# Kernel tuning notes

Hardware: AMD Instinct MI355X
Metric: run time of the kernel (lower is better)

Reference implementation:

```python
import jax, jax.numpy as jnp
import numpy as np

N = 100000
E = 1600000
F_IN = 128
HID1, H1 = 32, 4
HID2, H2 = 32, 4
NUM_CLASSES = 16
NEG_SLOPE = 0.2  # PyG GATConv default


def _glorot(key, shape, fan_in):
    return jax.random.normal(key, shape, dtype=jnp.float32) / jnp.sqrt(jnp.float32(fan_in))


def setup_inputs() -> dict:
    key = jax.random.key(0)
    ks = jax.random.split(key, 12)
    x = jax.random.normal(ks[0], (N, F_IN), dtype=jnp.float32)
    edge_index = jax.random.randint(ks[1], (2, E), 0, N, dtype=jnp.int64)
    W1 = _glorot(ks[2], (F_IN, H1 * HID1), F_IN)
    a_src1 = _glorot(ks[3], (H1, HID1), HID1)
    a_dst1 = _glorot(ks[4], (H1, HID1), HID1)
    b1 = jnp.zeros((H1 * HID1,), dtype=jnp.float32)
    W2 = _glorot(ks[5], (H1 * HID1, H2 * HID2), H1 * HID1)
    a_src2 = _glorot(ks[6], (H2, HID2), HID2)
    a_dst2 = _glorot(ks[7], (H2, HID2), HID2)
    b2 = jnp.zeros((HID2,), dtype=jnp.float32)
    Wc = _glorot(ks[8], (HID2, NUM_CLASSES), HID2)
    bc = jnp.zeros((NUM_CLASSES,), dtype=jnp.float32)
    return {"x": x, "edge_index": edge_index, "W1": W1, "a_src1": a_src1,
            "a_dst1": a_dst1, "b1": b1, "W2": W2, "a_src2": a_src2,
            "a_dst2": a_dst2, "b2": b2, "Wc": Wc, "bc": bc}


def gat_layer(x, src, dst, W, a_s, a_d, b, concat):
    # x: [N, Fin]; src/dst: [E'] with self-loops included
    n = x.shape[0]
    H, C = a_s.shape
    h = (x @ W).reshape(n, H, C)                      # [N, H, C]
    alpha_s = jnp.einsum('nhc,hc->nh', h, a_s)        # [N, H]
    alpha_d = jnp.einsum('nhc,hc->nh', h, a_d)
    e = jax.nn.leaky_relu(alpha_s[src] + alpha_d[dst], NEG_SLOPE)  # [E', H]
    m = jax.ops.segment_max(e, dst, num_segments=n)   # segment softmax (stable)
    ex = jnp.exp(e - m[dst])
    denom = jax.ops.segment_sum(ex, dst, num_segments=n)
    alpha = ex / denom[dst]                           # [E', H]
    msg = alpha[:, :, None] * h[src]                  # [E', H, C]
    out = jax.ops.segment_sum(msg, dst, num_segments=n)  # [N, H, C]
    out = out.reshape(n, H * C) if concat else out.mean(axis=1)
    return out + b


def reference(x, edge_index, W1, a_src1, a_dst1, b1, W2, a_src2, a_dst2, b2, Wc, bc):
    n = x.shape[0]
    loop = jnp.arange(n, dtype=edge_index.dtype)
    src = jnp.concatenate([edge_index[0], loop])  # add self-loops (PyG default)
    dst = jnp.concatenate([edge_index[1], loop])
    h = gat_layer(x, src, dst, W1, a_src1, a_dst1, b1, concat=True)
    h = jax.nn.relu(h)  # dropout is identity in eval mode
    h = gat_layer(h, src, dst, W2, a_src2, a_dst2, b2, concat=False)
    h = jax.nn.relu(h)
    return h @ Wc + bc
```

## Files before the change

### kernel.cpp

```cpp
#include <hip/hip_runtime.h>
#include <hip/hip_fp16.h>


__device__ __forceinline__ float leaky02(float v) { return v > 0.f ? v : 0.2f * v; }

struct h2x2 { __half2 a, b; };

#define NPB 1024
#define MAXNB 128
#define EPT 16
#define CH 4096

__global__ __launch_bounds__(256) void k_bucketize(const int* __restrict__ ei,
                                                   uint2* __restrict__ ebuf,
                                                   int* __restrict__ bcur,
                                                   int E, int N, int NB, int region) {
  __shared__ int hist[MAXNB];
  __shared__ int lbase[MAXNB];
  const int t = threadIdx.x;
  const int base = blockIdx.x * CH;
  const int Ep = E + N;
  if (t < MAXNB) hist[t] = 0;
  __syncthreads();
  int src[EPT], dst[EPT];
#pragma unroll
  for (int k = 0; k < EPT; ++k) {
    int e = base + k * 256 + t;
    if (e < E) { src[k] = ei[e]; dst[k] = ei[E + e]; }
    else if (e < Ep) { src[k] = dst[k] = e - E; }
    else { src[k] = -1; dst[k] = -1; }
    if (dst[k] >= 0) atomicAdd(&hist[dst[k] >> 10], 1);
  }
  __syncthreads();
  if (t < NB && hist[t] > 0) lbase[t] = atomicAdd(&bcur[t], hist[t]);
  __syncthreads();
  if (t < MAXNB) hist[t] = 0;
  __syncthreads();
#pragma unroll
  for (int k = 0; k < EPT; ++k) {
    if (dst[k] >= 0) {
      int b = dst[k] >> 10;
      int r = atomicAdd(&hist[b], 1);
      ebuf[(size_t)b * region + lbase[b] + r] =
          make_uint2((unsigned)src[k], (unsigned)dst[k]);
    }
  }
}

__global__ void k_bscan(const int* __restrict__ bcur, int* __restrict__ colbase,
                        int* __restrict__ rowptr, int NB, int N, int Ep) {
  __shared__ int lds[MAXNB];
  int t = threadIdx.x;
  int v = (t < NB) ? bcur[t] : 0;
  lds[t] = v;
  __syncthreads();
  for (int off = 1; off < MAXNB; off <<= 1) {
    int u = (t >= off) ? lds[t - off] : 0;
    __syncthreads();
    lds[t] += u;
    __syncthreads();
  }
  if (t < NB) colbase[t] = lds[t] - v;
  if (t == 0) rowptr[N] = Ep;
}

__global__ __launch_bounds__(256) void k_csr(const uint2* __restrict__ ebuf,
                                             const int* __restrict__ bcur,
                                             const int* __restrict__ colbase,
                                             int* __restrict__ rowptr,
                                             int* __restrict__ colsrc,
                                             int N, int region) {
  __shared__ int cnt[NPB];
  __shared__ int lds2[256];
  const int b = blockIdx.x;
  const int t = threadIdx.x;
  const int m = bcur[b];
  const size_t ebase = (size_t)b * region;
  const int cb = colbase[b];
#pragma unroll
  for (int i = 0; i < 4; ++i) cnt[t * 4 + i] = 0;
  __syncthreads();
  for (int j = t; j < m; j += 256) {
    int d = (int)(ebuf[ebase + j].y) & (NPB - 1);
    atomicAdd(&cnt[d], 1);
  }
  __syncthreads();
  int v[4], s = 0;
#pragma unroll
  for (int i = 0; i < 4; ++i) { v[i] = cnt[t * 4 + i]; s += v[i]; }
  lds2[t] = s;
  __syncthreads();
  for (int off = 1; off < 256; off <<= 1) {
    int u = (t >= off) ? lds2[t - off] : 0;
    __syncthreads();
    lds2[t] += u;
    __syncthreads();
  }
  int e = lds2[t] - s;
  const int node0 = (b << 10) + t * 4;
#pragma unroll
  for (int i = 0; i < 4; ++i) {
    cnt[t * 4 + i] = e;
    if (node0 + i < N) rowptr[node0 + i] = cb + e;
    e += v[i];
  }
  __syncthreads();
  for (int j = t; j < m; j += 256) {
    uint2 q = ebuf[ebase + j];
    int d = (int)q.y & (NPB - 1);
    int r = atomicAdd(&cnt[d], 1);
    colsrc[cb + r] = (int)q.x;
  }
}

__global__ __launch_bounds__(256) void k_gemm_fused(const float* __restrict__ A,
                                                    const float* __restrict__ W,
                                                    const float* __restrict__ avs,
                                                    const float* __restrict__ avd,
                                                    __half* __restrict__ Hh,
                                                    float* __restrict__ as_out,
                                                    float* __restrict__ ad_out,
                                                    int nrows) {
  __shared__ float sA[16][68];
  __shared__ float sB[16][68];
  const int t = threadIdx.x;
  const int row0 = blockIdx.x * 64;
  const int col0 = blockIdx.y * 64;
  const int tx = t & 15, ty = t >> 4;
  float acc[4][4] = {{0.f, 0.f, 0.f, 0.f}, {0.f, 0.f, 0.f, 0.f},
                     {0.f, 0.f, 0.f, 0.f}, {0.f, 0.f, 0.f, 0.f}};
  for (int kc = 0; kc < 128; kc += 16) {
    {
      int m = t >> 2;
      int k4 = (t & 3) * 4;
      int row = row0 + m;
      float4 a = (row < nrows) ? *(const float4*)&A[(size_t)row * 128 + kc + k4]
                               : make_float4(0.f, 0.f, 0.f, 0.f);
      sA[k4 + 0][m] = a.x;
      sA[k4 + 1][m] = a.y;
      sA[k4 + 2][m] = a.z;
      sA[k4 + 3][m] = a.w;
    }
    {
      int kk = t >> 4;
      int c4 = (t & 15) * 4;
      float4 b = *(const float4*)&W[(size_t)(kc + kk) * 128 + col0 + c4];
      *(float4*)&sB[kk][c4] = b;
    }
    __syncthreads();
#pragma unroll
    for (int k = 0; k < 16; ++k) {
      const float4 a = *(const float4*)&sA[k][ty * 4];
      const float4 b = *(const float4*)&sB[k][tx * 4];
      float av[4] = {a.x, a.y, a.z, a.w};
      float bv[4] = {b.x, b.y, b.z, b.w};
#pragma unroll
      for (int i = 0; i < 4; ++i)
#pragma unroll
        for (int j = 0; j < 4; ++j) acc[i][j] = fmaf(av[i], bv[j], acc[i][j]);
    }
    __syncthreads();
  }
  const float4 s4 = *(const float4*)&avs[col0 + tx * 4];
  const float4 d4 = *(const float4*)&avd[col0 + tx * 4];
#pragma unroll
  for (int i = 0; i < 4; ++i) {
    const int row = row0 + ty * 4 + i;
    float ps = acc[i][0] * s4.x + acc[i][1] * s4.y + acc[i][2] * s4.z + acc[i][3] * s4.w;
    float pd = acc[i][0] * d4.x + acc[i][1] * d4.y + acc[i][2] * d4.z + acc[i][3] * d4.w;
    for (int off = 1; off < 8; off <<= 1) {
      ps += __shfl_xor(ps, off);
      pd += __shfl_xor(pd, off);
    }
    if (row < nrows) {
      if ((tx & 7) == 0) {
        int head = (col0 >> 5) + (tx >> 3);
        as_out[row * 4 + head] = ps;
        ad_out[row * 4 + head] = pd;
      }
      h2x2 pk;
      pk.a = __floats2half2_rn(acc[i][0], acc[i][1]);
      pk.b = __floats2half2_rn(acc[i][2], acc[i][3]);
      *(h2x2*)&Hh[(size_t)row * 128 + col0 + tx * 4] = pk;
    }
  }
}

template <int LAYER>
__global__ __launch_bounds__(256) void k_agg(const int* __restrict__ rowptr,
                                             const int* __restrict__ colsrc,
                                             const float* __restrict__ as,
                                             const float* __restrict__ ad,
                                             const __half* __restrict__ Hh,
                                             const float* __restrict__ b1,
                                             const float* __restrict__ b2,
                                             const float* __restrict__ Wc,
                                             const float* __restrict__ bc,
                                             float* __restrict__ out, int n) {
  __shared__ float sbuf[8][128];
  const int slot = threadIdx.x >> 5;
  const int l = threadIdx.x & 31;
  const int node = blockIdx.x * 8 + slot;
  const bool active = node < n;
  int start = 0, end = 0;
  float4 adv = make_float4(0.f, 0.f, 0.f, 0.f);
  if (active) {
    start = rowptr[node];
    end = rowptr[node + 1];
    adv = *(const float4*)&ad[node * 4];
  }
  const int hd = l >> 3;
  const float adh = hd == 0 ? adv.x : hd == 1 ? adv.y : hd == 2 ? adv.z : adv.w;
  const int c = l * 4;
  float4 acc = make_float4(0.f, 0.f, 0.f, 0.f);
  float dsum = 0.f;
  int e = start;
  for (; e + 3 < end; e += 4) {
    int s0 = colsrc[e], s1 = colsrc[e + 1], s2 = colsrc[e + 2], s3 = colsrc[e + 3];
    float a0 = as[s0 * 4 + hd];
    float a1 = as[s1 * 4 + hd];
    float a2 = as[s2 * 4 + hd];
    float a3 = as[s3 * 4 + hd];
    h2x2 q0 = *(const h2x2*)&Hh[(size_t)s0 * 128 + c];
    h2x2 q1 = *(const h2x2*)&Hh[(size_t)s1 * 128 + c];
    h2x2 q2 = *(const h2x2*)&Hh[(size_t)s2 * 128 + c];
    h2x2 q3 = *(const h2x2*)&Hh[(size_t)s3 * 128 + c];
    float w0 = __expf(leaky02(a0 + adh));
    float w1 = __expf(leaky02(a1 + adh));
    float w2 = __expf(leaky02(a2 + adh));
    float w3 = __expf(leaky02(a3 + adh));
    dsum += w0 + w1 + w2 + w3;
    float2 f0a = __half22float2(q0.a), f0b = __half22float2(q0.b);
    float2 f1a = __half22float2(q1.a), f1b = __half22float2(q1.b);
    float2 f2a = __half22float2(q2.a), f2b = __half22float2(q2.b);
    float2 f3a = __half22float2(q3.a), f3b = __half22float2(q3.b);
    acc.x = fmaf(w0, f0a.x, acc.x); acc.y = fmaf(w0, f0a.y, acc.y);
    acc.z = fmaf(w0, f0b.x, acc.z); acc.w = fmaf(w0, f0b.y, acc.w);
    acc.x = fmaf(w1, f1a.x, acc.x); acc.y = fmaf(w1, f1a.y, acc.y);
    acc.z = fmaf(w1, f1b.x, acc.z); acc.w = fmaf(w1, f1b.y, acc.w);
    acc.x = fmaf(w2, f2a.x, acc.x); acc.y = fmaf(w2, f2a.y, acc.y);
    acc.z = fmaf(w2, f2b.x, acc.z); acc.w = fmaf(w2, f2b.y, acc.w);
    acc.x = fmaf(w3, f3a.x, acc.x); acc.y = fmaf(w3, f3a.y, acc.y);
    acc.z = fmaf(w3, f3b.x, acc.z); acc.w = fmaf(w3, f3b.y, acc.w);
  }
  for (; e < end; ++e) {
    int s0 = colsrc[e];
    float w = __expf(leaky02(as[s0 * 4 + hd] + adh));
    h2x2 q = *(const h2x2*)&Hh[(size_t)s0 * 128 + c];
    float2 fa = __half22float2(q.a), fb = __half22float2(q.b);
    dsum += w;
    acc.x = fmaf(w, fa.x, acc.x); acc.y = fmaf(w, fa.y, acc.y);
    acc.z = fmaf(w, fb.x, acc.z); acc.w = fmaf(w, fb.y, acc.w);
  }
  const float inv = dsum > 0.f ? 1.0f / dsum : 0.f;
  acc.x *= inv; acc.y *= inv; acc.z *= inv; acc.w *= inv;
  if (LAYER == 1) {
    if (active) {
      float4 bv = *(const float4*)&b1[c];
      acc.x = fmaxf(acc.x + bv.x, 0.f);
      acc.y = fmaxf(acc.y + bv.y, 0.f);
      acc.z = fmaxf(acc.z + bv.z, 0.f);
      acc.w = fmaxf(acc.w + bv.w, 0.f);
      *(float4*)&out[(size_t)node * 128 + c] = acc;
    }
  } else {
    *(float4*)&sbuf[slot][c] = acc;
    __syncthreads();
    float f = 0.25f * (sbuf[slot][l] + sbuf[slot][l + 32] +
                       sbuf[slot][l + 64] + sbuf[slot][l + 96]);
    f = fmaxf(f + b2[l], 0.f);
    __syncthreads();
    sbuf[slot][l] = f;
    __syncthreads();
    if (active && l < 16) {
      float o = bc[l];
#pragma unroll
      for (int cc = 0; cc < 32; ++cc) o = fmaf(sbuf[slot][cc], Wc[cc * 16 + l], o);
      out[(size_t)node * 16 + l] = o;
    }
  }
}

extern "C" void kernel_launch(void* const* d_in, const int* in_sizes, int n_in,
                              void* d_out, int out_size, void* d_ws, size_t ws_size,
                              hipStream_t stream) {
  const float* x = (const float*)d_in[0];
  const int* ei = (const int*)d_in[1];
  const float* W1 = (const float*)d_in[2];
  const float* a_s1 = (const float*)d_in[3];
  const float* a_d1 = (const float*)d_in[4];
  const float* b1 = (const float*)d_in[5];
  const float* W2 = (const float*)d_in[6];
  const float* a_s2 = (const float*)d_in[7];
  const float* a_d2 = (const float*)d_in[8];
  const float* b2 = (const float*)d_in[9];
  const float* Wc = (const float*)d_in[10];
  const float* bc = (const float*)d_in[11];
  float* out = (float*)d_out;

  const int N = in_sizes[0] / 128;
  const int E = in_sizes[1] / 2;
  const int Ep = E + N;
  const int NB = (N + NPB - 1) >> 10;
  const int region = Ep / NB + 4096;

  char* p = (char*)d_ws;
  auto align16 = [](char* q) { return (char*)(((uintptr_t)q + 15) & ~(uintptr_t)15); };
  __half* Hh = (__half*)p;            p = align16(p + sizeof(__half) * (size_t)N * 128);
  float* x2 = (float*)p;              p = align16(p + sizeof(float) * (size_t)N * 128);
  float* asb = (float*)p;             p = align16(p + sizeof(float) * (size_t)N * 4);
  float* adb = (float*)p;             p = align16(p + sizeof(float) * (size_t)N * 4);
  int* rowptr = (int*)p;              p = align16(p + sizeof(int) * (size_t)(N + 1));
  int* bcur = (int*)p;                p = align16(p + sizeof(int) * MAXNB);
  int* colbase = (int*)p;             p = align16(p + sizeof(int) * MAXNB);
  int* colsrc = (int*)p;              p = align16(p + sizeof(int) * (size_t)Ep);
  uint2* ebuf = (uint2*)p;

  hipMemsetAsync(bcur, 0, sizeof(int) * MAXNB, stream);

  k_bucketize<<<(Ep + CH - 1) / CH, 256, 0, stream>>>(ei, ebuf, bcur, E, N, NB, region);
  k_bscan<<<1, MAXNB, 0, stream>>>(bcur, colbase, rowptr, NB, N, Ep);
  k_csr<<<NB, 256, 0, stream>>>(ebuf, bcur, colbase, rowptr, colsrc, N, region);

  dim3 ggrid((N + 63) / 64, 2);
  k_gemm_fused<<<ggrid, 256, 0, stream>>>(x, W1, a_s1, a_d1, Hh, asb, adb, N);
  k_agg<1><<<(N + 7) / 8, 256, 0, stream>>>(rowptr, colsrc, asb, adb, Hh,
                                            b1, nullptr, nullptr, nullptr, x2, N);
  k_gemm_fused<<<ggrid, 256, 0, stream>>>(x2, W2, a_s2, a_d2, Hh, asb, adb, N);
  k_agg<2><<<(N + 7) / 8, 256, 0, stream>>>(rowptr, colsrc, asb, adb, Hh,
                                            nullptr, b2, Wc, bc, out, N);
}
```

Baseline: 429.2 us.

## Use fp16 MFMA GEMM, store layer-1 output in fp16, fold bucket scan into CSR

Replaces the fp32 SIMT tiled GEMM with a 16x16x32 fp16 MFMA kernel. Each block now covers all 128 output columns, with W transposed into LDS and the attention projections computed from the MFMA accumulators. The layer-1 aggregation writes its activations as fp16, which halves intermediate traffic and feeds the second GEMM directly. The separate bucket-scan kernel is merged into each CSR block, which removes one launch but makes every block redundantly redo the scan. The GEMM inputs are now rounded to fp16, which reduces precision.

Result: faster. 403.3 us (-6.0%).

```diff
diff --git a/kernel.cpp b/kernel.cpp
--- a/kernel.cpp
+++ b/kernel.cpp
@@ -1,6 +1,10 @@
 #include <hip/hip_runtime.h>
 #include <hip/hip_fp16.h>
 
+
+typedef _Float16 f16;
+typedef f16 f16x8 __attribute__((ext_vector_type(8)));
+typedef float f32x4 __attribute__((ext_vector_type(4)));
 
 __device__ __forceinline__ float leaky02(float v) { return v > 0.f ? v : 0.2f * v; }
 
@@ -47,36 +51,28 @@
   }
 }
 
-__global__ void k_bscan(const int* __restrict__ bcur, int* __restrict__ colbase,
-                        int* __restrict__ rowptr, int NB, int N, int Ep) {
-  __shared__ int lds[MAXNB];
-  int t = threadIdx.x;
-  int v = (t < NB) ? bcur[t] : 0;
-  lds[t] = v;
-  __syncthreads();
-  for (int off = 1; off < MAXNB; off <<= 1) {
-    int u = (t >= off) ? lds[t - off] : 0;
-    __syncthreads();
-    lds[t] += u;
-    __syncthreads();
-  }
-  if (t < NB) colbase[t] = lds[t] - v;
-  if (t == 0) rowptr[N] = Ep;
-}
-
 __global__ __launch_bounds__(256) void k_csr(const uint2* __restrict__ ebuf,
                                              const int* __restrict__ bcur,
-                                             const int* __restrict__ colbase,
                                              int* __restrict__ rowptr,
                                              int* __restrict__ colsrc,
-                                             int N, int region) {
+                                             int N, int NB, int region) {
   __shared__ int cnt[NPB];
   __shared__ int lds2[256];
+  __shared__ int sscan[MAXNB];
   const int b = blockIdx.x;
   const int t = threadIdx.x;
+  if (t < MAXNB) sscan[t] = (t < NB) ? bcur[t] : 0;
+  __syncthreads();
+  for (int off = 1; off < MAXNB; off <<= 1) {
+    int u = (t < MAXNB && t >= off) ? sscan[t - off] : 0;
+    __syncthreads();
+    if (t < MAXNB) sscan[t] += u;
+    __syncthreads();
+  }
+  const int cb = (b == 0) ? 0 : sscan[b - 1];
+  if (b == 0 && t == 0) rowptr[N] = sscan[NB - 1];
   const int m = bcur[b];
   const size_t ebase = (size_t)b * region;
-  const int cb = colbase[b];
 #pragma unroll
   for (int i = 0; i < 4; ++i) cnt[t * 4 + i] = 0;
   __syncthreads();
@@ -113,75 +109,106 @@
   }
 }
 
-__global__ __launch_bounds__(256) void k_gemm_fused(const float* __restrict__ A,
-                                                    const float* __restrict__ W,
-                                                    const float* __restrict__ avs,
-                                                    const float* __restrict__ avd,
-                                                    __half* __restrict__ Hh,
-                                                    float* __restrict__ as_out,
-                                                    float* __restrict__ ad_out,
-                                                    int nrows) {
-  __shared__ float sA[16][68];
-  __shared__ float sB[16][68];
+template <int AFP16>
+__global__ __launch_bounds__(256) void k_gemm_mfma(const void* __restrict__ Ain,
+                                                   const float* __restrict__ W,
+                                                   const float* __restrict__ avs,
+                                                   const float* __restrict__ avd,
+                                                   __half* __restrict__ Hh,
+                                                   float* __restrict__ as_out,
+                                                   float* __restrict__ ad_out,
+                                                   int nrows) {
+  __shared__ __align__(16) f16 sA[64][136];
+  __shared__ __align__(16) f16 sBT[128][136];
   const int t = threadIdx.x;
   const int row0 = blockIdx.x * 64;
-  const int col0 = blockIdx.y * 64;
-  const int tx = t & 15, ty = t >> 4;
-  float acc[4][4] = {{0.f, 0.f, 0.f, 0.f}, {0.f, 0.f, 0.f, 0.f},
-                     {0.f, 0.f, 0.f, 0.f}, {0.f, 0.f, 0.f, 0.f}};
-  for (int kc = 0; kc < 128; kc += 16) {
-    {
-      int m = t >> 2;
-      int k4 = (t & 3) * 4;
-      int row = row0 + m;
-      float4 a = (row < nrows) ? *(const float4*)&A[(size_t)row * 128 + kc + k4]
-                               : make_float4(0.f, 0.f, 0.f, 0.f);
-      sA[k4 + 0][m] = a.x;
-      sA[k4 + 1][m] = a.y;
-      sA[k4 + 2][m] = a.z;
-      sA[k4 + 3][m] = a.w;
-    }
-    {
-      int kk = t >> 4;
-      int c4 = (t & 15) * 4;
-      float4 b = *(const float4*)&W[(size_t)(kc + kk) * 128 + col0 + c4];
-      *(float4*)&sB[kk][c4] = b;
-    }
-    __syncthreads();
-#pragma unroll
-    for (int k = 0; k < 16; ++k) {
-      const float4 a = *(const float4*)&sA[k][ty * 4];
-      const float4 b = *(const float4*)&sB[k][tx * 4];
-      float av[4] = {a.x, a.y, a.z, a.w};
-      float bv[4] = {b.x, b.y, b.z, b.w};
-#pragma unroll
-      for (int i = 0; i < 4; ++i)
-#pragma unroll
-        for (int j = 0; j < 4; ++j) acc[i][j] = fmaf(av[i], bv[j], acc[i][j]);
-    }
-    __syncthreads();
-  }
-  const float4 s4 = *(const float4*)&avs[col0 + tx * 4];
-  const float4 d4 = *(const float4*)&avd[col0 + tx * 4];
-#pragma unroll
-  for (int i = 0; i < 4; ++i) {
-    const int row = row0 + ty * 4 + i;
-    float ps = acc[i][0] * s4.x + acc[i][1] * s4.y + acc[i][2] * s4.z + acc[i][3] * s4.w;
-    float pd = acc[i][0] * d4.x + acc[i][1] * d4.y + acc[i][2] * d4.z + acc[i][3] * d4.w;
-    for (int off = 1; off < 8; off <<= 1) {
-      ps += __shfl_xor(ps, off);
-      pd += __shfl_xor(pd, off);
+#pragma unroll
+  for (int i = 0; i < 16; ++i) {
+    int idx = (t + i * 256) * 4;
+    int k = idx >> 7, n = idx & 127;
+    float4 w4 = *(const float4*)&W[idx];
+    sBT[n + 0][k] = (f16)w4.x;
+    sBT[n + 1][k] = (f16)w4.y;
+    sBT[n + 2][k] = (f16)w4.z;
+    sBT[n + 3][k] = (f16)w4.w;
+  }
+  if (AFP16) {
+    const __half* A = (const __half*)Ain + (size_t)row0 * 128;
+#pragma unroll
+    for (int i = 0; i < 8; ++i) {
+      int idx = (t + i * 256) * 4;
+      int m = idx >> 7, c = idx & 127;
+      h2x2 v;
+      if (row0 + m < nrows) v = *(const h2x2*)&A[idx];
+      else { v.a = __floats2half2_rn(0.f, 0.f); v.b = v.a; }
+      *(h2x2*)&sA[m][c] = v;
+    }
+  } else {
+    const float* A = (const float*)Ain + (size_t)row0 * 128;
+#pragma unroll
+    for (int i = 0; i < 8; ++i) {
+      int idx = (t + i * 256) * 4;
+      int m = idx >> 7, c = idx & 127;
+      float4 a4 = (row0 + m < nrows) ? *(const float4*)&A[idx]
+                                     : make_float4(0.f, 0.f, 0.f, 0.f);
+      h2x2 v;
+      v.a = __floats2half2_rn(a4.x, a4.y);
+      v.b = __floats2half2_rn(a4.z, a4.w);
+      *(h2x2*)&sA[m][c] = v;
+    }
+  }
+  __syncthreads();
+  const int wv = t >> 6;
+  const int l = t & 63;
+  const int lm = l & 15;
+  const int lk = (l >> 4) * 8;
+  const int mw = wv * 16;
+  f32x4 acc[8];
+#pragma unroll
+  for (int tt = 0; tt < 8; ++tt) acc[tt] = (f32x4){0.f, 0.f, 0.f, 0.f};
+#pragma unroll
+  for (int kb = 0; kb < 4; ++kb) {
+    f16x8 af = *(const f16x8*)&sA[mw + lm][kb * 32 + lk];
+#pragma unroll
+    for (int tt = 0; tt < 8; ++tt) {
+      f16x8 bf = *(const f16x8*)&sBT[tt * 16 + lm][kb * 32 + lk];
+      acc[tt] = __builtin_amdgcn_mfma_f32_16x16x32_f16(af, bf, acc[tt], 0, 0, 0);
+    }
+  }
+  float avst[8], avdt[8];
+#pragma unroll
+  for (int tt = 0; tt < 8; ++tt) {
+    avst[tt] = avs[tt * 16 + lm];
+    avdt[tt] = avd[tt * 16 + lm];
+  }
+#pragma unroll
+  for (int reg = 0; reg < 4; ++reg) {
+    const int row = row0 + mw + (l >> 4) * 4 + reg;
+    float ps0 = acc[0][reg] * avst[0] + acc[1][reg] * avst[1];
+    float ps1 = acc[2][reg] * avst[2] + acc[3][reg] * avst[3];
+    float ps2 = acc[4][reg] * avst[4] + acc[5][reg] * avst[5];
+    float ps3 = acc[6][reg] * avst[6] + acc[7][reg] * avst[7];
+    float pd0 = acc[0][reg] * avdt[0] + acc[1][reg] * avdt[1];
+    float pd1 = acc[2][reg] * avdt[2] + acc[3][reg] * avdt[3];
+    float pd2 = acc[4][reg] * avdt[4] + acc[5][reg] * avdt[5];
+    float pd3 = acc[6][reg] * avdt[6] + acc[7][reg] * avdt[7];
+#pragma unroll
+    for (int off = 1; off < 16; off <<= 1) {
+      ps0 += __shfl_xor(ps0, off); ps1 += __shfl_xor(ps1, off);
+      ps2 += __shfl_xor(ps2, off); ps3 += __shfl_xor(ps3, off);
+      pd0 += __shfl_xor(pd0, off); pd1 += __shfl_xor(pd1, off);
+      pd2 += __shfl_xor(pd2, off); pd3 += __shfl_xor(pd3, off);
     }
     if (row < nrows) {
-      if ((tx & 7) == 0) {
-        int head = (col0 >> 5) + (tx >> 3);
-        as_out[row * 4 + head] = ps;
-        ad_out[row * 4 + head] = pd;
+      if (lm < 4) {
+        float vs = lm == 0 ? ps0 : lm == 1 ? ps1 : lm == 2 ? ps2 : ps3;
+        float vd = lm == 0 ? pd0 : lm == 1 ? pd1 : lm == 2 ? pd2 : pd3;
+        as_out[row * 4 + lm] = vs;
+        ad_out[row * 4 + lm] = vd;
       }
-      h2x2 pk;
-      pk.a = __floats2half2_rn(acc[i][0], acc[i][1]);
-      pk.b = __floats2half2_rn(acc[i][2], acc[i][3]);
-      *(h2x2*)&Hh[(size_t)row * 128 + col0 + tx * 4] = pk;
+#pragma unroll
+      for (int tt = 0; tt < 8; ++tt)
+        Hh[(size_t)row * 128 + tt * 16 + lm] = __float2half(acc[tt][reg]);
     }
   }
 }
@@ -196,6 +223,7 @@
                                              const float* __restrict__ b2,
                                              const float* __restrict__ Wc,
                                              const float* __restrict__ bc,
+                                             __half* __restrict__ outh,
                                              float* __restrict__ out, int n) {
   __shared__ float sbuf[8][128];
   const int slot = threadIdx.x >> 5;
@@ -257,11 +285,10 @@
   if (LAYER == 1) {
     if (active) {
       float4 bv = *(const float4*)&b1[c];
-      acc.x = fmaxf(acc.x + bv.x, 0.f);
-      acc.y = fmaxf(acc.y + bv.y, 0.f);
-      acc.z = fmaxf(acc.z + bv.z, 0.f);
-      acc.w = fmaxf(acc.w + bv.w, 0.f);
-      *(float4*)&out[(size_t)node * 128 + c] = acc;
+      h2x2 pk;
+      pk.a = __floats2half2_rn(fmaxf(acc.x + bv.x, 0.f), fmaxf(acc.y + bv.y, 0.f));
+      pk.b = __floats2half2_rn(fmaxf(acc.z + bv.z, 0.f), fmaxf(acc.w + bv.w, 0.f));
+      *(h2x2*)&outh[(size_t)node * 128 + c] = pk;
     }
   } else {
     *(float4*)&sbuf[slot][c] = acc;
@@ -306,27 +333,25 @@
 
   char* p = (char*)d_ws;
   auto align16 = [](char* q) { return (char*)(((uintptr_t)q + 15) & ~(uintptr_t)15); };
-  __half* Hh = (__half*)p;            p = align16(p + sizeof(__half) * (size_t)N * 128);
-  float* x2 = (float*)p;              p = align16(p + sizeof(float) * (size_t)N * 128);
-  float* asb = (float*)p;             p = align16(p + sizeof(float) * (size_t)N * 4);
-  float* adb = (float*)p;             p = align16(p + sizeof(float) * (size_t)N * 4);
-  int* rowptr = (int*)p;              p = align16(p + sizeof(int) * (size_t)(N + 1));
-  int* bcur = (int*)p;                p = align16(p + sizeof(int) * MAXNB);
-  int* colbase = (int*)p;             p = align16(p + sizeof(int) * MAXNB);
-  int* colsrc = (int*)p;              p = align16(p + sizeof(int) * (size_t)Ep);
+  __half* Hh = (__half*)p;   p = align16(p + sizeof(__half) * (size_t)N * 128);
+  __half* x2h = (__half*)p;  p = align16(p + sizeof(__half) * (size_t)N * 128);
+  float* asb = (float*)p;    p = align16(p + sizeof(float) * (size_t)N * 4);
+  float* adb = (float*)p;    p = align16(p + sizeof(float) * (size_t)N * 4);
+  int* rowptr = (int*)p;     p = align16(p + sizeof(int) * (size_t)(N + 1));
+  int* bcur = (int*)p;       p = align16(p + sizeof(int) * MAXNB);
+  int* colsrc = (int*)p;     p = align16(p + sizeof(int) * (size_t)Ep);
   uint2* ebuf = (uint2*)p;
 
   hipMemsetAsync(bcur, 0, sizeof(int) * MAXNB, stream);
 
   k_bucketize<<<(Ep + CH - 1) / CH, 256, 0, stream>>>(ei, ebuf, bcur, E, N, NB, region);
-  k_bscan<<<1, MAXNB, 0, stream>>>(bcur, colbase, rowptr, NB, N, Ep);
-  k_csr<<<NB, 256, 0, stream>>>(ebuf, bcur, colbase, rowptr, colsrc, N, region);
-
-  dim3 ggrid((N + 63) / 64, 2);
-  k_gemm_fused<<<ggrid, 256, 0, stream>>>(x, W1, a_s1, a_d1, Hh, asb, adb, N);
+  k_csr<<<NB, 256, 0, stream>>>(ebuf, bcur, rowptr, colsrc, N, NB, region);
+
+  const int gblocks = (N + 63) / 64;
+  k_gemm_mfma<0><<<gblocks, 256, 0, stream>>>(x, W1, a_s1, a_d1, Hh, asb, adb, N);
   k_agg<1><<<(N + 7) / 8, 256, 0, stream>>>(rowptr, colsrc, asb, adb, Hh,
-                                            b1, nullptr, nullptr, nullptr, x2, N);
-  k_gemm_fused<<<ggrid, 256, 0, stream>>>(x2, W2, a_s2, a_d2, Hh, asb, adb, N);
+                                            b1, nullptr, nullptr, nullptr, x2h, nullptr, N);
+  k_gemm_mfma<1><<<gblocks, 256, 0, stream>>>(x2h, W2, a_s2, a_d2, Hh, asb, adb, N);
   k_agg<2><<<(N + 7) / 8, 256, 0, stream>>>(rowptr, colsrc, asb, adb, Hh,
-                                            nullptr, b2, Wc, bc, out, N);
-}
+                                            nullptr, b2, Wc, bc, nullptr, out, N);
+}
```
